# Performance work log

Measured on AMD Instinct MI355X. Metric: run time of the kernel, lower is better.

## Reference

```python
import jax, jax.numpy as jnp
import numpy as np
from jax import lax

B, C, H, W = 64, 1, 256, 256
N = H * W
K = 16384  # positive_trials
LOG_CLAMP = -100.0  # torch BCELoss clamps log terms at -100


def setup_inputs() -> dict:
    key = jax.random.key(0)
    k1, k2, k3 = jax.random.split(key, 3)
    decision_scores = jax.random.normal(k1, (B, N, 2), dtype=jnp.float32)
    s_map = jax.random.uniform(k2, (B, C, H, W), dtype=jnp.float32)
    # gumbel noise g = -log(-log(U)), matching F.gumbel_softmax sampling
    u = jax.random.uniform(k3, (B, N, 2), dtype=jnp.float32, minval=1e-10, maxval=1.0)
    gumbel_noise = -jnp.log(-jnp.log(u))
    return {"decision_scores": decision_scores, "s_map": s_map, "gumbel_noise": gumbel_noise}


def reference(decision_scores, s_map, gumbel_noise):
    # Tokenizer: b c h w -> b (h w) c
    tokens = jnp.transpose(s_map.reshape(B, C, H * W), (0, 2, 1))  # [B, N, 1]
    # soft gumbel-softmax (tau=1, hard=False), keep prob of class 0
    soft = jax.nn.softmax(decision_scores + gumbel_noise, axis=-1)[:, :, 0:1]  # [B, N, 1]
    # top-K salient token indices per sample (descending sort -> top_k)
    _, idx = lax.top_k(tokens[:, :, 0], K)  # [B, K]
    trials = jnp.zeros((B, N), dtype=tokens.dtype)
    trials = trials.at[jnp.arange(B)[:, None], idx].set(1.0)[:, :, None]  # [B, N, 1]
    # BCE with reduction='sum', log clamped at -100 like torch
    log_p = jnp.clip(jnp.log(soft), LOG_CLAMP, None)
    log_1mp = jnp.clip(jnp.log(1.0 - soft), LOG_CLAMP, None)
    loss = -jnp.sum(trials * log_p + (1.0 - trials) * log_1mp)
    return loss
```

## Files before the change

### kernel.cpp

```cpp
#include <hip/hip_runtime.h>
#include <cstdint>

#define BATCH 64
#define NPIX 65536
#define TOPK 16384
#define NB 256
#define SEGS 32
#define WLO 186
#define WHI 198
#define NWBIN (WHI - WLO + 1)
#define CAPB 192
#define WCAP 4096
#define FCAP 1024

__device__ __forceinline__ float block_reduce(float acc) {
    __shared__ float w[4];
    __syncthreads();
    #pragma unroll
    for (int off = 32; off > 0; off >>= 1) acc += __shfl_down(acc, off, 64);
    if ((threadIdx.x & 63) == 0) w[threadIdx.x >> 6] = acc;
    __syncthreads();
    return w[0] + w[1] + w[2] + w[3];
}

__device__ __forceinline__ void bce_from_d(float d, float& lp, float& llp) {
    float t = __logf(1.f + __expf(-fabsf(d)));
    lp  = fmaxf(fminf(d, 0.f) - t, -100.f);
    llp = fmaxf(-fmaxf(d, 0.f) - t, -100.f);
}

__device__ __forceinline__ int vkey(float v) {
    return (int)fminf(v * 256.0f, 255.0f);
}

__global__ __launch_bounds__(256) void k1_pass(
    const float4* __restrict__ sc, const float4* __restrict__ gn,
    const float2* __restrict__ tokp,
    float* __restrict__ pk1, float* __restrict__ psel, float* __restrict__ phi,
    uint32_t* __restrict__ gcc,
    uint32_t* __restrict__ cvb, uint32_t* __restrict__ cvi,
    uint32_t* __restrict__ cvd, float* __restrict__ out)
{
    __shared__ uint32_t bvb[CAPB], bvi[CAPB], bvd[CAPB];
    __shared__ uint32_t ccount;
    const int tid = threadIdx.x;
    if (tid < CAPB) { bvb[tid] = 0u; bvi[tid] = 0u; bvd[tid] = 0u; }
    if (tid == 0) { ccount = 0u; if (blockIdx.x == 0) out[0] = 0.f; }
    __syncthreads();

    const int b   = blockIdx.x >> 5;
    const int seg = blockIdx.x & (SEGS - 1);
    const int pairbase = b * (NPIX / 2) + seg * 1024;
    float acc = 0.f, asel = 0.f, chi = 0.f;

    #pragma unroll
    for (int it = 0; it < 4; ++it) {
        int j = pairbase + it * 256 + tid;
        float4 s = sc[j];
        float4 g = gn[j];
        float2 tk = tokp[j];
        int px0 = (j - b * (NPIX / 2)) * 2;
        {
            float d = (s.x + g.x) - (s.y + g.y);
            float lp, llp; bce_from_d(d, lp, llp);
            acc += llp;
            float diff = lp - llp;
            int k = vkey(tk.x);
            if (k > WHI) { asel += diff; chi += 1.f; }
            else if (k >= WLO) {
                uint32_t p = atomicAdd(&ccount, 1u);
                if (p < CAPB) {
                    bvb[p] = __float_as_uint(tk.x);
                    bvi[p] = (uint32_t)px0;
                    bvd[p] = __float_as_uint(diff);
                }
            }
        }
        {
            float d = (s.z + g.z) - (s.w + g.w);
            float lp, llp; bce_from_d(d, lp, llp);
            acc += llp;
            float diff = lp - llp;
            int k = vkey(tk.y);
            if (k > WHI) { asel += diff; chi += 1.f; }
            else if (k >= WLO) {
                uint32_t p = atomicAdd(&ccount, 1u);
                if (p < CAPB) {
                    bvb[p] = __float_as_uint(tk.y);
                    bvi[p] = (uint32_t)(px0 + 1);
                    bvd[p] = __float_as_uint(diff);
                }
            }
        }
    }
    __syncthreads();
    const size_t cbase = (size_t)blockIdx.x * CAPB;
    if (tid < CAPB) {
        cvb[cbase + tid] = bvb[tid];
        cvi[cbase + tid] = bvi[tid];
        cvd[cbase + tid] = bvd[tid];
    }
    if (tid == 0) gcc[blockIdx.x] = ccount;

    float t1 = block_reduce(acc);
    float t2 = block_reduce(asel);
    float t3 = block_reduce(chi);
    if (tid == 0) {
        pk1[blockIdx.x]  = t1;
        psel[blockIdx.x] = t2;
        phi[blockIdx.x]  = t3;
    }
}

__global__ __launch_bounds__(256) void k4_finalize(
    const uint32_t* __restrict__ cvb, const uint32_t* __restrict__ cvi,
    const uint32_t* __restrict__ cvd, const uint32_t* __restrict__ gcc,
    const float* __restrict__ pk1, const float* __restrict__ psel,
    const float* __restrict__ phi,
    const float4* __restrict__ tok4,
    const float2* __restrict__ sc2, const float2* __restrict__ gn2,
    float* __restrict__ out)
{
    __shared__ uint32_t wcv[WCAP], wci[WCAP];
    __shared__ float    wcd[WCAP];
    __shared__ uint32_t fvb[FCAP], fvi[FCAP];
    __shared__ float    fdf[FCAP];
    __shared__ uint32_t fh[NB];
    __shared__ uint32_t wc[NWBIN];
    __shared__ uint32_t wcnt, fcnt;
    __shared__ int      sh_sb, sh_ovf;
    __shared__ uint32_t sh_rem;
    __shared__ float    shseg[SEGS];

    const int b = blockIdx.x, tid = threadIdx.x;
    if (tid == 0) { wcnt = 0u; fcnt = 0u; sh_ovf = 0; sh_sb = -1; sh_rem = 1u; }
    if (tid < NWBIN) wc[tid] = 0u;
    __syncthreads();

    const size_t base = (size_t)b * SEGS * CAPB;
    for (int t = tid; t < SEGS * CAPB; t += 256) {
        uint32_t vb = cvb[base + t];
        int k = vkey(__uint_as_float(vb));
        if (k >= WLO && k <= WHI) {
            uint32_t p = atomicAdd(&wcnt, 1u);
            if (p < WCAP) {
                wcv[p] = vb;
                wci[p] = cvi[base + t] & (NPIX - 1);
                wcd[p] = __uint_as_float(cvd[base + t]);
                atomicAdd(&wc[k - WLO], 1u);
            }
        }
    }
    if (tid < SEGS && gcc[b * SEGS + tid] > CAPB) sh_ovf = 1;
    if (tid < SEGS) shseg[tid] = phi[b * SEGS + tid];
    __syncthreads();

    if (tid == 0) {
        if (wcnt > WCAP) sh_ovf = 1;
        float chf = 0.f;
        for (int i = 0; i < SEGS; ++i) chf += shseg[i];
        uint32_t cnt_hi = (uint32_t)(chf + 0.5f);
        if (cnt_hi >= TOPK) sh_ovf = 1;
        else {
            uint32_t cum = cnt_hi;
            int found = -1; uint32_t rem = 1u;
            for (int j = WHI; j >= WLO; --j) {
                uint32_t nc = cum + wc[j - WLO];
                if (nc >= TOPK) { found = j; rem = TOPK - cum; break; }
                cum = nc;
            }
            if (found < 0) sh_ovf = 1;
            else { sh_sb = found; sh_rem = rem; }
        }
    }
    __syncthreads();
    bool fast = (sh_ovf == 0);
    int sb = sh_sb;
    float acc = 0.f;
    if (tid < SEGS) acc += pk1[b * SEGS + tid];

    if (fast) {
        if (tid < SEGS) acc += psel[b * SEGS + tid];
        uint32_t nstage = min(wcnt, (uint32_t)WCAP);
        for (uint32_t j = tid; j < nstage; j += 256) {
            int k = vkey(__uint_as_float(wcv[j]));
            if (k > sb) acc += wcd[j];
            else if (k == sb) {
                uint32_t p = atomicAdd(&fcnt, 1u);
                if (p < FCAP) { fvb[p] = wcv[j]; fvi[p] = wci[j]; fdf[p] = wcd[j]; }
            }
        }
        __syncthreads();
        if (fcnt > FCAP) fast = false;
        if (fast) {
            const uint32_t cnt = fcnt, rem = sh_rem;
            for (uint32_t j = tid; j < cnt; j += 256) {
                const uint32_t mb = fvb[j], mi = fvi[j];
                uint32_t rank = 0;
                for (uint32_t i = 0; i < cnt; ++i) {
                    uint32_t ob = fvb[i];
                    rank += (ob > mb) || (ob == mb && fvi[i] < mi);
                }
                if (rank < rem) acc += fdf[j];
            }
        }
    }

    if (!fast) {
        acc = (tid < SEGS) ? pk1[b * SEGS + tid] : 0.f;
        for (int i = tid; i < NB; i += 256) fh[i] = 0u;
        if (tid == 0) fcnt = 0u;
        __syncthreads();
        const float4* tbase = tok4 + (size_t)b * (NPIX / 4);
        for (int it = 0; it < 64; ++it) {
            float4 v = tbase[it * 256 + tid];
            atomicAdd(&fh[vkey(v.x)], 1u);
            atomicAdd(&fh[vkey(v.y)], 1u);
            atomicAdd(&fh[vkey(v.z)], 1u);
            atomicAdd(&fh[vkey(v.w)], 1u);
        }
        __syncthreads();
        if (tid == 0) {
            uint32_t cum = 0; int bin = NB - 1;
            for (; bin > 0; --bin) {
                if (cum + fh[bin] >= TOPK) break;
                cum += fh[bin];
            }
            sh_sb = bin; sh_rem = TOPK - cum;
        }
        __syncthreads();
        const int sb2 = sh_sb; const uint32_t rem2 = sh_rem;
        for (int it = 0; it < 64; ++it) {
            int j = it * 256 + tid;
            float4 v = tbase[j];
            int px = j * 4;
            float fv[4] = {v.x, v.y, v.z, v.w};
            #pragma unroll
            for (int q = 0; q < 4; ++q) {
                int k = vkey(fv[q]);
                if (k > sb2) {
                    size_t idx = (size_t)b * NPIX + (px + q);
                    float2 S = sc2[idx]; float2 G = gn2[idx];
                    float d = (S.x + G.x) - (S.y + G.y);
                    float lp, llp; bce_from_d(d, lp, llp);
                    acc += lp - llp;
                } else if (k == sb2) {
                    uint32_t p = atomicAdd(&fcnt, 1u);
                    if (p < FCAP) { fvb[p] = __float_as_uint(fv[q]); fvi[p] = (uint32_t)(px + q); }
                }
            }
        }
        __syncthreads();
        const uint32_t cnt2 = min(fcnt, (uint32_t)FCAP);
        for (uint32_t j = tid; j < cnt2; j += 256) {
            const uint32_t mb = fvb[j], mi = fvi[j];
            uint32_t rank = 0;
            for (uint32_t i = 0; i < cnt2; ++i) {
                uint32_t ob = fvb[i];
                rank += (ob > mb) || (ob == mb && fvi[i] < mi);
            }
            if (rank < rem2) {
                size_t idx = (size_t)b * NPIX + (mi & (NPIX - 1));
                float2 S = sc2[idx]; float2 G = gn2[idx];
                float d = (S.x + G.x) - (S.y + G.y);
                float lp, llp; bce_from_d(d, lp, llp);
                acc += lp - llp;
            }
        }
    }

    float tot = block_reduce(acc);
    if (tid == 0) atomicAdd(out, -tot);
}

extern "C" void kernel_launch(void* const* d_in, const int* in_sizes, int n_in,
                              void* d_out, int out_size, void* d_ws, size_t ws_size,
                              hipStream_t stream) {
    const float* scores = (const float*)d_in[0];
    const float* smap   = (const float*)d_in[1];
    const float* gumbel = (const float*)d_in[2];
    float* out = (float*)d_out;

    char* ws = (char*)d_ws;
    float*    pk1  = (float*)ws;     ws += (size_t)BATCH * SEGS * 4;
    float*    psel = (float*)ws;     ws += (size_t)BATCH * SEGS * 4;
    float*    phi  = (float*)ws;     ws += (size_t)BATCH * SEGS * 4;
    uint32_t* gcc  = (uint32_t*)ws;  ws += (size_t)BATCH * SEGS * 4;
    uint32_t* cvb  = (uint32_t*)ws;  ws += (size_t)BATCH * SEGS * CAPB * 4;
    uint32_t* cvi  = (uint32_t*)ws;  ws += (size_t)BATCH * SEGS * CAPB * 4;
    uint32_t* cvd  = (uint32_t*)ws;  ws += (size_t)BATCH * SEGS * CAPB * 4;

    k1_pass<<<BATCH * SEGS, 256, 0, stream>>>(
        (const float4*)scores, (const float4*)gumbel, (const float2*)smap,
        pk1, psel, phi, gcc, cvb, cvi, cvd, out);

    k4_finalize<<<BATCH, 256, 0, stream>>>(
        cvb, cvi, cvd, gcc, pk1, psel, phi,
        (const float4*)smap, (const float2*)scores, (const float2*)gumbel, out);
}
```

Baseline: 136.3 us.

## Fuse finalize into main pass via last-block-per-batch atomic counter

Merges the two kernels into one: each block atomically increments a per-batch counter, and the last of the 32 segment blocks for a batch does the top-K threshold and selection work. A global finish counter then lets the last batch block sum the per-batch totals deterministically into the output. The large shared staging window is removed; the finalize step re-reads candidates from global memory, and the bin window and per-block candidate capacity shrink. This aims to cut a kernel launch and the tail of the second grid, at the cost of an extra memset, threadfences, and a serialized tail on whichever block finishes last.

```diff
diff --git a/kernel.cpp b/kernel.cpp
--- a/kernel.cpp
+++ b/kernel.cpp
@@ -6,12 +6,12 @@
 #define TOPK 16384
 #define NB 256
 #define SEGS 32
-#define WLO 186
-#define WHI 198
+#define WLO 187
+#define WHI 197
 #define NWBIN (WHI - WLO + 1)
-#define CAPB 192
-#define WCAP 4096
+#define CAPB 176
 #define FCAP 1024
+#define CNT_STRIDE 16
 
 __device__ __forceinline__ float block_reduce(float acc) {
     __shared__ float w[4];
@@ -33,19 +33,30 @@
     return (int)fminf(v * 256.0f, 255.0f);
 }
 
-__global__ __launch_bounds__(256) void k1_pass(
+__global__ __launch_bounds__(256) void fused_kernel(
     const float4* __restrict__ sc, const float4* __restrict__ gn,
     const float2* __restrict__ tokp,
+    const float4* __restrict__ tok4,
+    const float2* __restrict__ sc2, const float2* __restrict__ gn2,
     float* __restrict__ pk1, float* __restrict__ psel, float* __restrict__ phi,
     uint32_t* __restrict__ gcc,
     uint32_t* __restrict__ cvb, uint32_t* __restrict__ cvi,
-    uint32_t* __restrict__ cvd, float* __restrict__ out)
+    uint32_t* __restrict__ cvd,
+    uint32_t* __restrict__ bcnt, uint32_t* __restrict__ fin_cnt,
+    float* __restrict__ pbatch, float* __restrict__ out)
 {
     __shared__ uint32_t bvb[CAPB], bvi[CAPB], bvd[CAPB];
-    __shared__ uint32_t ccount;
+    __shared__ uint32_t fvb[FCAP], fvi[FCAP];
+    __shared__ float    fdf[FCAP];
+    __shared__ uint32_t wc[NWBIN];
+    __shared__ uint32_t fh[NB];
+    __shared__ uint32_t ccount, fcnt;
+    __shared__ int      sh_sb, sh_ovf, sh_last;
+    __shared__ uint32_t sh_rem;
+
     const int tid = threadIdx.x;
     if (tid < CAPB) { bvb[tid] = 0u; bvi[tid] = 0u; bvd[tid] = 0u; }
-    if (tid == 0) { ccount = 0u; if (blockIdx.x == 0) out[0] = 0.f; }
+    if (tid == 0) ccount = 0u;
     __syncthreads();
 
     const int b   = blockIdx.x >> 5;
@@ -110,63 +121,39 @@
         psel[blockIdx.x] = t2;
         phi[blockIdx.x]  = t3;
     }
-}
-
-__global__ __launch_bounds__(256) void k4_finalize(
-    const uint32_t* __restrict__ cvb, const uint32_t* __restrict__ cvi,
-    const uint32_t* __restrict__ cvd, const uint32_t* __restrict__ gcc,
-    const float* __restrict__ pk1, const float* __restrict__ psel,
-    const float* __restrict__ phi,
-    const float4* __restrict__ tok4,
-    const float2* __restrict__ sc2, const float2* __restrict__ gn2,
-    float* __restrict__ out)
-{
-    __shared__ uint32_t wcv[WCAP], wci[WCAP];
-    __shared__ float    wcd[WCAP];
-    __shared__ uint32_t fvb[FCAP], fvi[FCAP];
-    __shared__ float    fdf[FCAP];
-    __shared__ uint32_t fh[NB];
-    __shared__ uint32_t wc[NWBIN];
-    __shared__ uint32_t wcnt, fcnt;
-    __shared__ int      sh_sb, sh_ovf;
-    __shared__ uint32_t sh_rem;
-    __shared__ float    shseg[SEGS];
-
-    const int b = blockIdx.x, tid = threadIdx.x;
-    if (tid == 0) { wcnt = 0u; fcnt = 0u; sh_ovf = 0; sh_sb = -1; sh_rem = 1u; }
+
+    __syncthreads();
+    if (tid == 0) {
+        __threadfence();
+        uint32_t oldc = atomicAdd(&bcnt[b * CNT_STRIDE], 1u);
+        sh_last = (oldc == SEGS - 1) ? 1 : 0;
+    }
+    __syncthreads();
+    if (!sh_last) return;
+    __threadfence();
+
     if (tid < NWBIN) wc[tid] = 0u;
+    if (tid == 0) { fcnt = 0u; sh_sb = -1; sh_ovf = 0; sh_rem = 1u; }
     __syncthreads();
 
     const size_t base = (size_t)b * SEGS * CAPB;
     for (int t = tid; t < SEGS * CAPB; t += 256) {
         uint32_t vb = cvb[base + t];
         int k = vkey(__uint_as_float(vb));
-        if (k >= WLO && k <= WHI) {
-            uint32_t p = atomicAdd(&wcnt, 1u);
-            if (p < WCAP) {
-                wcv[p] = vb;
-                wci[p] = cvi[base + t] & (NPIX - 1);
-                wcd[p] = __uint_as_float(cvd[base + t]);
-                atomicAdd(&wc[k - WLO], 1u);
-            }
-        }
+        if (k >= WLO && k <= WHI) atomicAdd(&wc[k - WLO], 1u);
     }
     if (tid < SEGS && gcc[b * SEGS + tid] > CAPB) sh_ovf = 1;
-    if (tid < SEGS) shseg[tid] = phi[b * SEGS + tid];
-    __syncthreads();
-
+    float chl = (tid < SEGS) ? phi[b * SEGS + tid] : 0.f;
+    float chf = block_reduce(chl);
     if (tid == 0) {
-        if (wcnt > WCAP) sh_ovf = 1;
-        float chf = 0.f;
-        for (int i = 0; i < SEGS; ++i) chf += shseg[i];
         uint32_t cnt_hi = (uint32_t)(chf + 0.5f);
         if (cnt_hi >= TOPK) sh_ovf = 1;
         else {
             uint32_t cum = cnt_hi;
             int found = -1; uint32_t rem = 1u;
-            for (int j = WHI; j >= WLO; --j) {
-                uint32_t nc = cum + wc[j - WLO];
-                if (nc >= TOPK) { found = j; rem = TOPK - cum; break; }
+            for (int jj = WHI; jj >= WLO; --jj) {
+                uint32_t nc = cum + wc[jj - WLO];
+                if (nc >= TOPK) { found = jj; rem = TOPK - cum; break; }
                 cum = nc;
             }
             if (found < 0) sh_ovf = 1;
@@ -174,20 +161,24 @@
         }
     }
     __syncthreads();
+
     bool fast = (sh_ovf == 0);
-    int sb = sh_sb;
-    float acc = 0.f;
-    if (tid < SEGS) acc += pk1[b * SEGS + tid];
+    const int sb = sh_sb;
+    float fac = (tid < SEGS) ? pk1[b * SEGS + tid] : 0.f;
 
     if (fast) {
-        if (tid < SEGS) acc += psel[b * SEGS + tid];
-        uint32_t nstage = min(wcnt, (uint32_t)WCAP);
-        for (uint32_t j = tid; j < nstage; j += 256) {
-            int k = vkey(__uint_as_float(wcv[j]));
-            if (k > sb) acc += wcd[j];
+        if (tid < SEGS) fac += psel[b * SEGS + tid];
+        for (int t = tid; t < SEGS * CAPB; t += 256) {
+            uint32_t vb = cvb[base + t];
+            int k = vkey(__uint_as_float(vb));
+            if (k > sb) fac += __uint_as_float(cvd[base + t]);
             else if (k == sb) {
                 uint32_t p = atomicAdd(&fcnt, 1u);
-                if (p < FCAP) { fvb[p] = wcv[j]; fvi[p] = wci[j]; fdf[p] = wcd[j]; }
+                if (p < FCAP) {
+                    fvb[p] = vb;
+                    fvi[p] = cvi[base + t] & (NPIX - 1);
+                    fdf[p] = __uint_as_float(cvd[base + t]);
+                }
             }
         }
         __syncthreads();
@@ -201,13 +192,13 @@
                     uint32_t ob = fvb[i];
                     rank += (ob > mb) || (ob == mb && fvi[i] < mi);
                 }
-                if (rank < rem) acc += fdf[j];
+                if (rank < rem) fac += fdf[j];
             }
         }
     }
 
     if (!fast) {
-        acc = (tid < SEGS) ? pk1[b * SEGS + tid] : 0.f;
+        fac = (tid < SEGS) ? pk1[b * SEGS + tid] : 0.f;
         for (int i = tid; i < NB; i += 256) fh[i] = 0u;
         if (tid == 0) fcnt = 0u;
         __syncthreads();
@@ -243,7 +234,7 @@
                     float2 S = sc2[idx]; float2 G = gn2[idx];
                     float d = (S.x + G.x) - (S.y + G.y);
                     float lp, llp; bce_from_d(d, lp, llp);
-                    acc += lp - llp;
+                    fac += lp - llp;
                 } else if (k == sb2) {
                     uint32_t p = atomicAdd(&fcnt, 1u);
                     if (p < FCAP) { fvb[p] = __float_as_uint(fv[q]); fvi[p] = (uint32_t)(px + q); }
@@ -264,13 +255,23 @@
                 float2 S = sc2[idx]; float2 G = gn2[idx];
                 float d = (S.x + G.x) - (S.y + G.y);
                 float lp, llp; bce_from_d(d, lp, llp);
-                acc += lp - llp;
-            }
-        }
-    }
-
-    float tot = block_reduce(acc);
-    if (tid == 0) atomicAdd(out, -tot);
+                fac += lp - llp;
+            }
+        }
+    }
+
+    float tot = block_reduce(fac);
+    if (tid == 0) {
+        pbatch[b] = tot;
+        __threadfence();
+        uint32_t f = atomicAdd(fin_cnt, 1u);
+        if (f == BATCH - 1) {
+            __threadfence();
+            float sum = 0.f;
+            for (int i = 0; i < BATCH; ++i) sum += pbatch[i];
+            out[0] = -sum;
+        }
+    }
 }
 
 extern "C" void kernel_launch(void* const* d_in, const int* in_sizes, int n_in,
@@ -282,19 +283,21 @@
     float* out = (float*)d_out;
 
     char* ws = (char*)d_ws;
-    float*    pk1  = (float*)ws;     ws += (size_t)BATCH * SEGS * 4;
-    float*    psel = (float*)ws;     ws += (size_t)BATCH * SEGS * 4;
-    float*    phi  = (float*)ws;     ws += (size_t)BATCH * SEGS * 4;
-    uint32_t* gcc  = (uint32_t*)ws;  ws += (size_t)BATCH * SEGS * 4;
-    uint32_t* cvb  = (uint32_t*)ws;  ws += (size_t)BATCH * SEGS * CAPB * 4;
-    uint32_t* cvi  = (uint32_t*)ws;  ws += (size_t)BATCH * SEGS * CAPB * 4;
-    uint32_t* cvd  = (uint32_t*)ws;  ws += (size_t)BATCH * SEGS * CAPB * 4;
-
-    k1_pass<<<BATCH * SEGS, 256, 0, stream>>>(
+    float*    pk1    = (float*)ws;     ws += (size_t)BATCH * SEGS * 4;
+    float*    psel   = (float*)ws;     ws += (size_t)BATCH * SEGS * 4;
+    float*    phi    = (float*)ws;     ws += (size_t)BATCH * SEGS * 4;
+    uint32_t* gcc    = (uint32_t*)ws;  ws += (size_t)BATCH * SEGS * 4;
+    uint32_t* cvb    = (uint32_t*)ws;  ws += (size_t)BATCH * SEGS * CAPB * 4;
+    uint32_t* cvi    = (uint32_t*)ws;  ws += (size_t)BATCH * SEGS * CAPB * 4;
+    uint32_t* cvd    = (uint32_t*)ws;  ws += (size_t)BATCH * SEGS * CAPB * 4;
+    float*    pbatch = (float*)ws;     ws += (size_t)BATCH * 4;
+    uint32_t* bcnt   = (uint32_t*)ws;
+    uint32_t* fin    = bcnt + BATCH * CNT_STRIDE;
+
+    hipMemsetAsync(bcnt, 0, (size_t)(BATCH * CNT_STRIDE + 16) * 4, stream);
+
+    fused_kernel<<<BATCH * SEGS, 256, 0, stream>>>(
         (const float4*)scores, (const float4*)gumbel, (const float2*)smap,
-        pk1, psel, phi, gcc, cvb, cvi, cvd, out);
-
-    k4_finalize<<<BATCH, 256, 0, stream>>>(
-        cvb, cvi, cvd, gcc, pk1, psel, phi,
-        (const float4*)smap, (const float2*)scores, (const float2*)gumbel, out);
-}
+        (const float4*)smap, (const float2*)scores, (const float2*)gumbel,
+        pk1, psel, phi, gcc, cvb, cvi, cvd, bcnt, fin, pbatch, out);
+}
```

Result: slower. 226.1 us (+65.9%).
